# Kernel optimization log

Hardware: AMD Instinct MI355X
Metric: run time of the kernel (lower is better)

## Reference

```python
import jax, jax.numpy as jnp
import numpy as np

KS = 2          # kernel_size
ITERS = 3       # iterations
EPS = 1e-5


def _unfold(x, k):
    # non-overlapping unfold (stride == kernel): (B,C,H,W) -> (B,C,k*k,T)
    B, C, H, W = x.shape
    x = x.reshape(B, C, H // k, k, W // k, k)
    x = x.transpose(0, 1, 3, 5, 2, 4)           # B,C,kh,kw,Ho,Wo
    return x.reshape(B, C, k * k, (H // k) * (W // k))


def _fold(x, H, W, k):
    # inverse of _unfold: (B, C*k*k, T) -> (B,C,H,W)
    B, CKK, T = x.shape
    C = CKK // (k * k)
    x = x.reshape(B, C, k, k, H // k, W // k)
    x = x.transpose(0, 1, 4, 2, 5, 3)            # B,C,Ho,kh,Wo,kw
    return x.reshape(B, C, H, W)


def _ln_channel(x, g, b):
    # LayerNormDim1: LayerNorm over the channel dim (axis=1) of (B,C,H,W)
    mu = jnp.mean(x, axis=1, keepdims=True)
    var = jnp.var(x, axis=1, keepdims=True)
    xn = (x - mu) * jax.lax.rsqrt(var + EPS)
    return xn * g[None, :, None, None] + b[None, :, None, None]


def setup_inputs() -> dict:
    key = jax.random.key(0)
    ks = jax.random.split(key, 7)
    B, f_in, H, W = 4, 256, 128, 128
    f_out = 512
    s = 0.02
    f32 = jnp.float32
    return {
        "x_in": jax.random.normal(ks[0], (B, f_in, H, W), f32),
        "conv_w": jax.random.normal(ks[1], (f_out, f_in, KS, KS), f32) * s,
        "conv_b": jnp.zeros((f_out,), f32),
        "k_w": jax.random.normal(ks[2], (f_out, f_in), f32) * s,
        "k_b": jnp.zeros((f_out,), f32),
        "q_w": jax.random.normal(ks[3], (f_out, f_out), f32) * s,
        "q_b": jnp.zeros((f_out,), f32),
        "v_w": jax.random.normal(ks[4], (f_out, f_in), f32) * s,
        "v_b": jnp.zeros((f_out,), f32),
        "mlp_w": jax.random.normal(ks[5], (f_out, f_out), f32) * s,
        "mlp_b": jnp.zeros((f_out,), f32),
        "lnc_g": jnp.ones((f_out,), f32),
        "lnc_b": jnp.zeros((f_out,), f32),
        "lnv_g": jnp.ones((f_out,), f32),
        "lnv_b": jnp.zeros((f_out,), f32),
        "lnm_g": jnp.ones((f_out,), f32),
        "lnm_b": jnp.zeros((f_out,), f32),
    }


def reference(x_in, conv_w, conv_b, k_w, k_b, q_w, q_b, v_w, v_b,
              mlp_w, mlp_b, lnc_g, lnc_b, lnv_g, lnv_b, lnm_g, lnm_b):
    temp = 1.0
    B, f_in, H, W = x_in.shape
    f_out = conv_w.shape[0]
    WIN = KS * KS
    Ho, Wo = H // KS, W // KS
    T_out = Ho * Wo

    # patchify conv (stride == kernel) + channel LayerNorm
    xc = jax.lax.conv_general_dilated(
        x_in, conv_w, window_strides=(KS, KS), padding="VALID",
        dimension_numbers=("NCHW", "OIHW", "NCHW"))
    x_out = _ln_channel(xc + conv_b[None, :, None, None], lnc_g, lnc_b)

    # k, v projections on the full-resolution input
    k = jnp.einsum("bihw,oi->bohw", x_in, k_w) + k_b[None, :, None, None]
    v = jnp.einsum("bihw,oi->bohw", x_in, v_w) + v_b[None, :, None, None]

    k_wins = _unfold(k, KS)

    for _ in range(ITERS):
        q = jnp.einsum("bihw,oi->bohw", x_out, q_w) + q_b[None, :, None, None]
        q = q.reshape(B, f_out, T_out)
        att = jnp.einsum("bfwt,bft->bwt", k_wins, q)
        att = jax.nn.softmax(att * temp, axis=1)
        att_map = _fold(att, H, W, KS)                   # (B, 1, H, W)
        update = v * att_map                             # broadcast over channels
        update = _unfold(update, KS).sum(axis=2)         # (B, f_out, T_out)
        update = update.reshape(B, f_out, Ho, Wo)
        x_out = x_out + _ln_channel(update, lnv_g, lnv_b)
        mlp = jnp.einsum("bihw,oi->bohw", x_out, mlp_w) + mlp_b[None, :, None, None]
        x_out = x_out + _ln_channel(mlp, lnm_g, lnm_b)

    return x_out
```

## Files before the change

kernel.cpp:

```cpp
#include <hip/hip_runtime.h>

#define NB 4
#define CIN 256
#define CO 512
#define HH 128
#define WW 128
#define PP (HH*WW)
#define HO 64
#define TT (HO*HO)
#define EPSL 1e-5f

typedef unsigned short u16;
typedef unsigned int   u32;
typedef __attribute__((ext_vector_type(8))) short short8;
typedef __attribute__((ext_vector_type(4))) short short4v;
typedef __attribute__((ext_vector_type(4))) float f32x4;

__device__ __forceinline__ float b2f(u16 u){
  union{float f; u32 i;} x; x.i = ((u32)u)<<16; return x.f;
}
__device__ __forceinline__ u16 f2b(float f){
  union{float f; u32 i;} x; x.f = f;
  u32 r = x.i + 0x7fffu + ((x.i>>16)&1u);
  return (u16)(r>>16);
}

__device__ __forceinline__ void gl16(const u16* g, u16* l){
  __builtin_amdgcn_global_load_lds((const __attribute__((address_space(1))) void*)g,
                                   (__attribute__((address_space(3))) void*)l, 16, 0, 0);
}

template<int K, int EPI>
__global__ __launch_bounds__(256) void gemm_t(
    const u16* __restrict__ Ah, const u16* __restrict__ Al, size_t aBS,
    const u16* __restrict__ Bh, const u16* __restrict__ Bl, size_t bBS,
    const float* __restrict__ bias,
    float* __restrict__ OUTf, u16* __restrict__ OPh, u16* __restrict__ OPl,
    size_t oBS, int oLd)
{
  const int z = blockIdx.z;
  const int r0 = blockIdx.x*128, c0 = blockIdx.y*128;
  const int tid = threadIdx.x, wid = tid>>6, lane = tid&63;
  const int wm = wid>>1, wn = wid&1, lr = lane&15, lg = lane>>4;

  extern __shared__ u16 sm[];

  const size_t abase = (size_t)z*aBS + (size_t)r0*K;
  const size_t bbase = (size_t)z*bBS + (size_t)c0*K;

  f32x4 acc[4][4] = {};

  const int q0 = tid, q1 = tid+256;
  const int r_0 = q0>>2, c_0 = q0&3;
  const int r_1 = q1>>2, c_1 = q1&3;
  const size_t go0 = (size_t)r_0*K + (size_t)((c_0 ^ ((r_0>>1)&3))*8);
  const size_t go1 = (size_t)r_1*K + (size_t)((c_1 ^ ((r_1>>1)&3))*8);

  const int NS = K/32;
  #pragma unroll 1
  for (int s = 0; s < NS; ++s) {
    if (s == 0) {
      u16* buf = sm;
      gl16(Ah+abase+go0, buf+q0*8);        gl16(Ah+abase+go1, buf+q1*8);
      gl16(Al+abase+go0, buf+4096+q0*8);   gl16(Al+abase+go1, buf+4096+q1*8);
      gl16(Bh+bbase+go0, buf+8192+q0*8);   gl16(Bh+bbase+go1, buf+8192+q1*8);
      gl16(Bl+bbase+go0, buf+12288+q0*8);  gl16(Bl+bbase+go1, buf+12288+q1*8);
    }
    if (s+1 < NS) {
      u16* buf = sm + ((s+1)&1)*16384;
      const size_t ko = (size_t)(s+1)*32;
      gl16(Ah+abase+go0+ko, buf+q0*8);        gl16(Ah+abase+go1+ko, buf+q1*8);
      gl16(Al+abase+go0+ko, buf+4096+q0*8);   gl16(Al+abase+go1+ko, buf+4096+q1*8);
      gl16(Bh+bbase+go0+ko, buf+8192+q0*8);   gl16(Bh+bbase+go1+ko, buf+8192+q1*8);
      gl16(Bl+bbase+go0+ko, buf+12288+q0*8);  gl16(Bl+bbase+go1+ko, buf+12288+q1*8);
      asm volatile("s_waitcnt vmcnt(8)" ::: "memory");
    } else {
      asm volatile("s_waitcnt vmcnt(0)" ::: "memory");
    }
    __builtin_amdgcn_s_barrier();
    __builtin_amdgcn_sched_barrier(0);
    {
      const u16* buf = sm + (s&1)*16384;
      const u16* Ax = buf, *Ay = buf+4096, *Bx = buf+8192, *By = buf+12288;
      short8 bh[4], bl[4];
      #pragma unroll
      for (int nf=0; nf<4; ++nf) {
        int row = wn*64 + nf*16 + lr;
        int off = row*32 + ((lg ^ ((row>>1)&3))<<3);
        bh[nf] = *(const short8*)(Bx+off);
        bl[nf] = *(const short8*)(By+off);
      }
      #pragma unroll
      for (int mf=0; mf<4; ++mf) {
        int row = wm*64 + mf*16 + lr;
        int off = row*32 + ((lg ^ ((row>>1)&3))<<3);
        short8 ah = *(const short8*)(Ax+off);
        short8 al = *(const short8*)(Ay+off);
        #pragma unroll
        for (int nf=0; nf<4; ++nf) {
          acc[mf][nf] = __builtin_amdgcn_mfma_f32_16x16x32_bf16(ah, bh[nf], acc[mf][nf],0,0,0);
          acc[mf][nf] = __builtin_amdgcn_mfma_f32_16x16x32_bf16(ah, bl[nf], acc[mf][nf],0,0,0);
          acc[mf][nf] = __builtin_amdgcn_mfma_f32_16x16x32_bf16(al, bh[nf], acc[mf][nf],0,0,0);
        }
      }
    }
    __builtin_amdgcn_sched_barrier(0);
    __builtin_amdgcn_s_barrier();
  }
  __builtin_amdgcn_sched_barrier(0);

  #pragma unroll
  for (int mf=0; mf<4; ++mf) {
    #pragma unroll
    for (int nf=0; nf<4; ++nf) {
      int col = c0 + wn*64 + nf*16 + lr;
      #pragma unroll
      for (int j=0; j<4; ++j) {
        int row = r0 + wm*64 + mf*16 + lg*4 + j;
        float v = acc[mf][nf][j] + (EPI==0 ? bias[row] : bias[col]);
        size_t oi = (size_t)z*oBS + (size_t)row*oLd + col;
        if (EPI==0) {
          OUTf[oi] = v;
        } else {
          u16 h = f2b(v);
          OPh[oi] = h;
          OPl[oi] = f2b(v - b2f(h));
        }
      }
    }
  }
}

template<int ADD>
__global__ __launch_bounds__(256) void ln_split(
    const u16* __restrict__ TPh, const u16* __restrict__ TPl,
    const float* __restrict__ g, const float* __restrict__ be,
    u16* __restrict__ XSh, u16* __restrict__ XSl)
{
  const int wid = threadIdx.x>>6, lane = threadIdx.x&63;
  const size_t row = (size_t)blockIdx.x*4 + wid;
  const size_t base = row*CO + lane*8;
  short8 h8 = *(const short8*)(TPh + base);
  short8 l8 = *(const short8*)(TPl + base);
  float v[8]; float s=0.f, s2=0.f;
  #pragma unroll
  for (int e=0;e<8;++e){ v[e]=b2f((u16)h8[e])+b2f((u16)l8[e]); s+=v[e]; s2+=v[e]*v[e]; }
  #pragma unroll
  for (int m=1;m<64;m<<=1){ s+=__shfl_xor(s,m,64); s2+=__shfl_xor(s2,m,64); }
  float mu = s*(1.f/CO);
  float rstd = rsqrtf(s2*(1.f/CO) - mu*mu + EPSL);
  const int cc0 = lane*8;
  float4 g0 = *(const float4*)(g+cc0), g1 = *(const float4*)(g+cc0+4);
  float4 e0 = *(const float4*)(be+cc0), e1 = *(const float4*)(be+cc0+4);
  float gg[8] = {g0.x,g0.y,g0.z,g0.w,g1.x,g1.y,g1.z,g1.w};
  float bb[8] = {e0.x,e0.y,e0.z,e0.w,e1.x,e1.y,e1.z,e1.w};
  short8 xh, xl;
  if (ADD) { xh = *(const short8*)(XSh+base); xl = *(const short8*)(XSl+base); }
  short8 oh, ol;
  #pragma unroll
  for (int e=0;e<8;++e){
    float r = gg[e]*(v[e]-mu)*rstd + bb[e];
    float nv = ADD ? (b2f((u16)xh[e]) + b2f((u16)xl[e]) + r) : r;
    u16 h = f2b(nv); oh[e]=(short)h; ol[e]=(short)f2b(nv - b2f(h));
  }
  *(short8*)(XSh+base) = oh;
  *(short8*)(XSl+base) = ol;
}

__global__ __launch_bounds__(256) void att_xp(
    const float* __restrict__ qk, const float* __restrict__ x_in,
    u16* __restrict__ XPh, u16* __restrict__ XPl)
{
  const int b = blockIdx.y;
  const int tl = threadIdx.x & 63, cg = threadIdx.x >> 6;
  const int t = blockIdx.x*64 + tl;
  const int ho = t >> 6, wo = t & 63;
  const size_t p00 = (size_t)(2*ho)*WW + 2*wo;

  float a0=0.f, a1=0.f, a2=0.f, a3=0.f;
  for (int i = cg*64; i < cg*64 + 64; ++i) {
    float qv = qk[((size_t)b*CIN + i)*TT + t];
    const float* xr = x_in + ((size_t)b*CIN + i)*PP + p00;
    float2 x01 = *(const float2*)xr;
    float2 x23 = *(const float2*)(xr + WW);
    a0 += qv*x01.x; a1 += qv*x01.y; a2 += qv*x23.x; a3 += qv*x23.y;
  }
  __shared__ float attp[4][64][4];
  attp[cg][tl][0] = a0; attp[cg][tl][1] = a1;
  attp[cg][tl][2] = a2; attp[cg][tl][3] = a3;
  __syncthreads();
  a0 = attp[0][tl][0] + attp[1][tl][0] + attp[2][tl][0] + attp[3][tl][0];
  a1 = attp[0][tl][1] + attp[1][tl][1] + attp[2][tl][1] + attp[3][tl][1];
  a2 = attp[0][tl][2] + attp[1][tl][2] + attp[2][tl][2] + attp[3][tl][2];
  a3 = attp[0][tl][3] + attp[1][tl][3] + attp[2][tl][3] + attp[3][tl][3];
  float m = fmaxf(fmaxf(a0,a1), fmaxf(a2,a3));
  float ee0 = __expf(a0-m), ee1 = __expf(a1-m), ee2 = __expf(a2-m), ee3 = __expf(a3-m);
  float inv = 1.f/(ee0+ee1+ee2+ee3);
  float p0 = ee0*inv, p1 = ee1*inv, p2 = ee2*inv, p3 = ee3*inv;

  for (int ib = 0; ib < 64; ib += 8) {
    short8 oh, ol;
    #pragma unroll
    for (int e = 0; e < 8; ++e) {
      int i = cg*64 + ib + e;
      const float* xr = x_in + ((size_t)b*CIN + i)*PP + p00;
      float2 x01 = *(const float2*)xr;
      float2 x23 = *(const float2*)(xr + WW);
      float u = p0*x01.x + p1*x01.y + p2*x23.x + p3*x23.y;
      u16 h = f2b(u); oh[e] = (short)h; ol[e] = (short)f2b(u - b2f(h));
    }
    size_t o = ((size_t)b*TT + t)*CIN + cg*64 + ib;
    *(short8*)(XPh + o) = oh;
    *(short8*)(XPl + o) = ol;
  }
}

__global__ __launch_bounds__(256) void xc_build(
    const float* __restrict__ x_in, u16* __restrict__ XCh, u16* __restrict__ XCl)
{
  const int ho = blockIdx.x, iblk = blockIdx.y, b = blockIdx.z;
  const int tid = threadIdx.x;
  __shared__ float Ls[32][256];
  {
    const int ii = tid >> 3, q = tid & 7;
    const float4* src = (const float4*)(x_in + ((size_t)(b*CIN + iblk*32 + ii)*PP + (size_t)ho*256));
    #pragma unroll
    for (int p = 0; p < 8; ++p) {
      float4 v = src[q + p*8];
      *(float4*)&Ls[ii][(q + p*8)*4] = v;
    }
  }
  __syncthreads();
  {
    const int wo = tid >> 2, w = tid & 3;
    const int colbase = (w>>1)*128 + 2*wo + (w&1);
    u16 hb[32], lb[32];
    #pragma unroll
    for (int ii = 0; ii < 32; ++ii) {
      float v = Ls[ii][colbase];
      u16 h = f2b(v); hb[ii] = h; lb[ii] = f2b(v - b2f(h));
    }
    size_t t = (size_t)b*TT + ho*64 + wo;
    size_t dst = t*1024 + (size_t)w*256 + iblk*32;
    #pragma unroll
    for (int c = 0; c < 4; ++c) {
      short8 hv, lv;
      #pragma unroll
      for (int e = 0; e < 8; ++e) { hv[e] = (short)hb[c*8+e]; lv[e] = (short)lb[c*8+e]; }
      *(short8*)(XCh + dst + c*8) = hv;
      *(short8*)(XCl + dst + c*8) = lv;
    }
  }
}

__global__ __launch_bounds__(256) void out_transpose(
    const u16* __restrict__ XSh, const u16* __restrict__ XSl, float* __restrict__ xout)
{
  const int b = blockIdx.z, c0 = blockIdx.y*64, t0l = blockIdx.x*64;
  const int tid = threadIdx.x;
  __shared__ float Ts[64][68];
  #pragma unroll
  for (int p = 0; p < 2; ++p) {
    int idx = tid + p*256;
    int row = idx >> 3, ko = (idx & 7)*8;
    size_t off = ((size_t)b*TT + t0l + row)*CO + c0 + ko;
    short8 h8 = *(const short8*)(XSh + off);
    short8 l8 = *(const short8*)(XSl + off);
    #pragma unroll
    for (int e = 0; e < 8; ++e)
      Ts[ko + e][row] = b2f((u16)h8[e]) + b2f((u16)l8[e]);
  }
  __syncthreads();
  const int cl = tid >> 2, tq = tid & 3;
  #pragma unroll
  for (int p = 0; p < 4; ++p) {
    int t4 = (tq + p*4)*4;
    float4 v = *(const float4*)&Ts[cl][t4];
    *(float4*)(xout + ((size_t)b*CO + c0 + cl)*TT + t0l + t4) = v;
  }
}

__global__ void split_pack(const float* __restrict__ src, u16* __restrict__ h,
                           u16* __restrict__ l, int n){
  int i = blockIdx.x*256 + threadIdx.x;
  if (i < n) { float v = src[i]; u16 hh = f2b(v); h[i]=hh; l[i]=f2b(v - b2f(hh)); }
}

__global__ void conv_pack(const float* __restrict__ cw, u16* __restrict__ h,
                          u16* __restrict__ l){
  int e = blockIdx.x*256 + threadIdx.x;
  int o = e >> 10, r = e & 1023, w = r >> 8, i = r & 255;
  float v = cw[o*1024 + i*4 + w];
  u16 hh = f2b(v); h[e]=hh; l[e]=f2b(v - b2f(hh));
}

__global__ __launch_bounds__(256) void gemm_tn(
    const float* __restrict__ A, const float* __restrict__ B,
    u16* __restrict__ MtH, u16* __restrict__ MtL)
{
  const int i0 = blockIdx.y*64, j0 = blockIdx.x*64;
  const int tid = threadIdx.x, tx = tid & 15, ty = tid >> 4;
  __shared__ float As[16][64];
  __shared__ float Bs[16][64];
  float acc[4][4] = {};
  for (int f0 = 0; f0 < CO; f0 += 16) {
    int tt = tid & 63, kkb = tid >> 6;
    #pragma unroll
    for (int s = 0; s < 4; ++s) {
      As[kkb+s*4][tt] = A[(size_t)(f0+kkb+s*4)*CIN + i0 + tt];
      Bs[kkb+s*4][tt] = B[(size_t)(f0+kkb+s*4)*CO  + j0 + tt];
    }
    __syncthreads();
    #pragma unroll
    for (int kk = 0; kk < 16; ++kk) {
      float4 av = *reinterpret_cast<const float4*>(&As[kk][ty*4]);
      float4 bv = *reinterpret_cast<const float4*>(&Bs[kk][tx*4]);
      float a[4] = {av.x,av.y,av.z,av.w}, c[4] = {bv.x,bv.y,bv.z,bv.w};
      #pragma unroll
      for (int j = 0; j < 4; ++j)
        #pragma unroll
        for (int i = 0; i < 4; ++i) acc[j][i] += a[j]*c[i];
    }
    __syncthreads();
  }
  #pragma unroll
  for (int j = 0; j < 4; ++j) {
    #pragma unroll
    for (int i = 0; i < 4; ++i) {
      float v = acc[j][i];
      size_t idx = (size_t)(i0+ty*4+j)*CO + j0 + tx*4 + i;
      u16 h = f2b(v);
      MtH[idx] = h; MtL[idx] = f2b(v - b2f(h));
    }
  }
}

__global__ void qbk_kernel(const float* __restrict__ q_b,
                           const float* __restrict__ k_w, float* __restrict__ qbk)
{
  int i = threadIdx.x;
  float s = 0.f;
  for (int f = 0; f < CO; ++f) s += q_b[f]*k_w[(size_t)f*CIN + i];
  qbk[i] = s;
}

extern "C" void kernel_launch(void* const* d_in, const int* in_sizes, int n_in,
                              void* d_out, int out_size, void* d_ws, size_t ws_size,
                              hipStream_t stream) {
  const float* x_in   = (const float*)d_in[0];
  const float* conv_w = (const float*)d_in[1];
  const float* conv_b = (const float*)d_in[2];
  const float* k_w    = (const float*)d_in[3];
  const float* q_w    = (const float*)d_in[5];
  const float* q_b    = (const float*)d_in[6];
  const float* v_w    = (const float*)d_in[7];
  const float* v_b    = (const float*)d_in[8];
  const float* mlp_w  = (const float*)d_in[9];
  const float* mlp_b  = (const float*)d_in[10];
  const float* lnc_g  = (const float*)d_in[11];
  const float* lnc_b  = (const float*)d_in[12];
  const float* lnv_g  = (const float*)d_in[13];
  const float* lnv_b  = (const float*)d_in[14];
  const float* lnm_g  = (const float*)d_in[15];
  const float* lnm_b  = (const float*)d_in[16];
  float* x_out = (float*)d_out;

  char* ws = (char*)d_ws;
  const size_t MBy = (size_t)1<<20;
  u16* XCh = (u16*)(ws + 0*MBy);
  u16* XCl = (u16*)(ws + 32*MBy);
  u16* XSh = (u16*)(ws + 0*MBy);
  u16* XSl = (u16*)(ws + 16*MBy);
  u16* XPh = (u16*)(ws + 32*MBy);
  u16* XPl = (u16*)(ws + 40*MBy);
  float* QK = (float*)(ws + 48*MBy);
  u16* TPh = (u16*)(ws + 64*MBy);
  u16* TPl = (u16*)(ws + 80*MBy);
  u16* WCh = (u16*)(ws + 96*MBy);
  u16* WCl = (u16*)(ws + 97*MBy);
  u16* MWh = (u16*)(ws + 98*MBy);
  u16* MWl = (u16*)(ws + 98*MBy + 512*1024);
  u16* VWh = (u16*)(ws + 99*MBy);
  u16* VWl = (u16*)(ws + 99*MBy + 256*1024);
  u16* MtH = (u16*)(ws + 99*MBy + 512*1024);
  u16* MtL = (u16*)(ws + 99*MBy + 768*1024);
  float* QBK = (float*)(ws + 100*MBy);

  conv_pack<<<2048, 256, 0, stream>>>(conv_w, WCh, WCl);
  split_pack<<<512, 256, 0, stream>>>(v_w, VWh, VWl, CO*CIN);
  split_pack<<<1024, 256, 0, stream>>>(mlp_w, MWh, MWl, CO*CO);
  gemm_tn<<<dim3(CO/64, CIN/64), 256, 0, stream>>>(k_w, q_w, MtH, MtL);
  qbk_kernel<<<1, CIN, 0, stream>>>(q_b, k_w, QBK);
  xc_build<<<dim3(HO, 8, NB), 256, 0, stream>>>(x_in, XCh, XCl);

  gemm_t<1024,1><<<dim3(TT/128, 4, NB), 256, 65536, stream>>>(
      XCh, XCl, (size_t)TT*1024, WCh, WCl, (size_t)0, conv_b,
      nullptr, TPh, TPl, (size_t)TT*CO, CO);
  ln_split<0><<<NB*TT/4, 256, 0, stream>>>(TPh, TPl, lnc_g, lnc_b, XSh, XSl);

  for (int it = 0; it < 3; ++it) {
    gemm_t<512,0><<<dim3(CIN/128, TT/128, NB), 256, 65536, stream>>>(
        MtH, MtL, (size_t)0, XSh, XSl, (size_t)TT*CO, QBK,
        QK, nullptr, nullptr, (size_t)CIN*TT, TT);
    att_xp<<<dim3(TT/64, NB), 256, 0, stream>>>(QK, x_in, XPh, XPl);
    gemm_t<256,1><<<dim3(TT/128, 4, NB), 256, 65536, stream>>>(
        XPh, XPl, (size_t)TT*CIN, VWh, VWl, (size_t)0, v_b,
        nullptr, TPh, TPl, (size_t)TT*CO, CO);
    ln_split<1><<<NB*TT/4, 256, 0, stream>>>(TPh, TPl, lnv_g, lnv_b, XSh, XSl);
    gemm_t<512,1><<<dim3(TT/128, 4, NB), 256, 65536, stream>>>(
        XSh, XSl, (size_t)TT*CO, MWh, MWl, (size_t)0, mlp_b,
        nullptr, TPh, TPl, (size_t)TT*CO, CO);
    ln_split<1><<<NB*TT/4, 256, 0, stream>>>(TPh, TPl, lnm_g, lnm_b, XSh, XSl);
  }

  out_transpose<<<dim3(TT/64, CO/64, NB), 256, 0, stream>>>(XSh, XSl, x_out);
}
```

Measured before the change: 719.0 us.

## Fuse channel LayerNorm into GEMM epilogue with full-row 64x512 tiles

```diff
diff --git a/kernel.cpp b/kernel.cpp
--- a/kernel.cpp
+++ b/kernel.cpp
@@ -8,12 +8,12 @@
 #define PP (HH*WW)
 #define HO 64
 #define TT (HO*HO)
+#define MTOT (NB*TT)
 #define EPSL 1e-5f
 
 typedef unsigned short u16;
 typedef unsigned int   u32;
 typedef __attribute__((ext_vector_type(8))) short short8;
-typedef __attribute__((ext_vector_type(4))) short short4v;
 typedef __attribute__((ext_vector_type(4))) float f32x4;
 
 __device__ __forceinline__ float b2f(u16 u){
@@ -30,13 +30,169 @@
                                    (__attribute__((address_space(3))) void*)l, 16, 0, 0);
 }
 
-template<int K, int EPI>
+template<int K, int MODE>
+__global__ __launch_bounds__(512) void gemm_ln64(
+    const u16* __restrict__ Ah, const u16* __restrict__ Al,
+    const u16* __restrict__ Bh, const u16* __restrict__ Bl,
+    const float* __restrict__ bias,
+    const float* __restrict__ g, const float* __restrict__ be,
+    u16* __restrict__ XSh, u16* __restrict__ XSl)
+{
+  const int r0 = blockIdx.x*64;
+  const int tid = threadIdx.x, wid = tid>>6, lane = tid&63;
+  const int lr = lane&15, lg = lane>>4;
+
+  __shared__ u16 smAh[2][2048];
+  __shared__ u16 smAl[2][2048];
+  __shared__ u16 smBh[2][16384];
+  __shared__ u16 smBl[2][16384];
+  __shared__ float red[2][64][8];
+
+  const size_t abase = (size_t)r0*K;
+  f32x4 acc[4][4] = {};
+
+  const int ach = tid & 255;
+  const int ar = ach>>2, ac = ach&3;
+  const size_t agoff = (size_t)ar*K + (size_t)((ac ^ ((ar>>1)&3))*8);
+  const u16* Aptr = (tid < 256 ? Ah : Al);
+  int brow[4]; size_t bgoff[4];
+  #pragma unroll
+  for (int p=0;p<4;++p){
+    int cb = p*512 + tid;
+    brow[p] = cb>>2; int bc = cb&3;
+    bgoff[p] = (size_t)brow[p]*K + (size_t)((bc ^ ((brow[p]>>1)&3))*8);
+  }
+
+  const int NS = K/32;
+  #pragma unroll 1
+  for (int s = 0; s < NS; ++s) {
+    if (s == 0) {
+      u16* a_d = (tid<256 ? smAh[0] : smAl[0]);
+      gl16(Aptr+abase+agoff, a_d + ach*8);
+      #pragma unroll
+      for (int p=0;p<4;++p){
+        int cb = p*512 + tid;
+        gl16(Bh+bgoff[p], smBh[0] + cb*8);
+        gl16(Bl+bgoff[p], smBl[0] + cb*8);
+      }
+    }
+    if (s+1 < NS) {
+      const int nb = (s+1)&1;
+      const size_t ko = (size_t)(s+1)*32;
+      u16* a_d = (tid<256 ? smAh[nb] : smAl[nb]);
+      gl16(Aptr+abase+agoff+ko, a_d + ach*8);
+      #pragma unroll
+      for (int p=0;p<4;++p){
+        int cb = p*512 + tid;
+        gl16(Bh+bgoff[p]+ko, smBh[nb] + cb*8);
+        gl16(Bl+bgoff[p]+ko, smBl[nb] + cb*8);
+      }
+      asm volatile("s_waitcnt vmcnt(9)" ::: "memory");
+    } else {
+      asm volatile("s_waitcnt vmcnt(0)" ::: "memory");
+    }
+    __builtin_amdgcn_s_barrier();
+    __builtin_amdgcn_sched_barrier(0);
+    {
+      const int bs = s&1;
+      short8 bhf[4], blf[4];
+      #pragma unroll
+      for (int nf=0; nf<4; ++nf) {
+        int row = wid*64 + nf*16 + lr;
+        int off = row*32 + ((lg ^ ((row>>1)&3))<<3);
+        bhf[nf] = *(const short8*)(smBh[bs]+off);
+        blf[nf] = *(const short8*)(smBl[bs]+off);
+      }
+      #pragma unroll
+      for (int mf=0; mf<4; ++mf) {
+        int row = mf*16 + lr;
+        int off = row*32 + ((lg ^ ((row>>1)&3))<<3);
+        short8 ah = *(const short8*)(smAh[bs]+off);
+        short8 al = *(const short8*)(smAl[bs]+off);
+        #pragma unroll
+        for (int nf=0; nf<4; ++nf) {
+          acc[mf][nf] = __builtin_amdgcn_mfma_f32_16x16x32_bf16(ah, bhf[nf], acc[mf][nf],0,0,0);
+          acc[mf][nf] = __builtin_amdgcn_mfma_f32_16x16x32_bf16(ah, blf[nf], acc[mf][nf],0,0,0);
+          acc[mf][nf] = __builtin_amdgcn_mfma_f32_16x16x32_bf16(al, bhf[nf], acc[mf][nf],0,0,0);
+        }
+      }
+    }
+    __builtin_amdgcn_sched_barrier(0);
+    __builtin_amdgcn_s_barrier();
+  }
+  __builtin_amdgcn_sched_barrier(0);
+
+  float s1[4][4] = {}, s2v[4][4] = {};
+  #pragma unroll
+  for (int nf=0; nf<4; ++nf) {
+    float bs = bias[wid*64 + nf*16 + lr];
+    #pragma unroll
+    for (int mf=0; mf<4; ++mf)
+      #pragma unroll
+      for (int j=0; j<4; ++j) {
+        float v = acc[mf][nf][j] + bs;
+        acc[mf][nf][j] = v;
+        s1[mf][j] += v; s2v[mf][j] += v*v;
+      }
+  }
+  #pragma unroll
+  for (int m=1; m<=8; m<<=1)
+    #pragma unroll
+    for (int mf=0; mf<4; ++mf)
+      #pragma unroll
+      for (int j=0; j<4; ++j) {
+        s1[mf][j]  += __shfl_xor(s1[mf][j],  m, 64);
+        s2v[mf][j] += __shfl_xor(s2v[mf][j], m, 64);
+      }
+  if (lr == 0) {
+    #pragma unroll
+    for (int mf=0; mf<4; ++mf)
+      #pragma unroll
+      for (int j=0; j<4; ++j) {
+        int row = mf*16 + lg*4 + j;
+        red[0][row][wid] = s1[mf][j];
+        red[1][row][wid] = s2v[mf][j];
+      }
+  }
+  __syncthreads();
+  float mu[4][4], rs[4][4];
+  #pragma unroll
+  for (int mf=0; mf<4; ++mf)
+    #pragma unroll
+    for (int j=0; j<4; ++j) {
+      int row = mf*16 + lg*4 + j;
+      float S = 0.f, S2 = 0.f;
+      #pragma unroll
+      for (int w=0; w<8; ++w) { S += red[0][row][w]; S2 += red[1][row][w]; }
+      float m_ = S*(1.f/CO);
+      mu[mf][j] = m_;
+      rs[mf][j] = rsqrtf(S2*(1.f/CO) - m_*m_ + EPSL);
+    }
+  #pragma unroll
+  for (int nf=0; nf<4; ++nf) {
+    int col = wid*64 + nf*16 + lr;
+    float gg = g[col], bb = be[col];
+    #pragma unroll
+    for (int mf=0; mf<4; ++mf)
+      #pragma unroll
+      for (int j=0; j<4; ++j) {
+        size_t grow = (size_t)r0 + mf*16 + lg*4 + j;
+        size_t xi = grow*CO + col;
+        float r = gg*(acc[mf][nf][j]-mu[mf][j])*rs[mf][j] + bb;
+        float nv = MODE ? (b2f(XSh[xi]) + b2f(XSl[xi]) + r) : r;
+        u16 h = f2b(nv);
+        XSh[xi] = h;
+        XSl[xi] = f2b(nv - b2f(h));
+      }
+  }
+}
+
+template<int K>
 __global__ __launch_bounds__(256) void gemm_t(
     const u16* __restrict__ Ah, const u16* __restrict__ Al, size_t aBS,
     const u16* __restrict__ Bh, const u16* __restrict__ Bl, size_t bBS,
     const float* __restrict__ bias,
-    float* __restrict__ OUTf, u16* __restrict__ OPh, u16* __restrict__ OPl,
-    size_t oBS, int oLd)
+    float* __restrict__ OUTf, size_t oBS, int oLd)
 {
   const int z = blockIdx.z;
   const int r0 = blockIdx.x*128, c0 = blockIdx.y*128;
@@ -117,54 +273,10 @@
       #pragma unroll
       for (int j=0; j<4; ++j) {
         int row = r0 + wm*64 + mf*16 + lg*4 + j;
-        float v = acc[mf][nf][j] + (EPI==0 ? bias[row] : bias[col]);
-        size_t oi = (size_t)z*oBS + (size_t)row*oLd + col;
-        if (EPI==0) {
-          OUTf[oi] = v;
-        } else {
-          u16 h = f2b(v);
-          OPh[oi] = h;
-          OPl[oi] = f2b(v - b2f(h));
-        }
-      }
-    }
-  }
-}
-
-template<int ADD>
-__global__ __launch_bounds__(256) void ln_split(
-    const u16* __restrict__ TPh, const u16* __restrict__ TPl,
-    const float* __restrict__ g, const float* __restrict__ be,
-    u16* __restrict__ XSh, u16* __restrict__ XSl)
-{
-  const int wid = threadIdx.x>>6, lane = threadIdx.x&63;
-  const size_t row = (size_t)blockIdx.x*4 + wid;
-  const size_t base = row*CO + lane*8;
-  short8 h8 = *(const short8*)(TPh + base);
-  short8 l8 = *(const short8*)(TPl + base);
-  float v[8]; float s=0.f, s2=0.f;
-  #pragma unroll
-  for (int e=0;e<8;++e){ v[e]=b2f((u16)h8[e])+b2f((u16)l8[e]); s+=v[e]; s2+=v[e]*v[e]; }
-  #pragma unroll
-  for (int m=1;m<64;m<<=1){ s+=__shfl_xor(s,m,64); s2+=__shfl_xor(s2,m,64); }
-  float mu = s*(1.f/CO);
-  float rstd = rsqrtf(s2*(1.f/CO) - mu*mu + EPSL);
-  const int cc0 = lane*8;
-  float4 g0 = *(const float4*)(g+cc0), g1 = *(const float4*)(g+cc0+4);
-  float4 e0 = *(const float4*)(be+cc0), e1 = *(const float4*)(be+cc0+4);
-  float gg[8] = {g0.x,g0.y,g0.z,g0.w,g1.x,g1.y,g1.z,g1.w};
-  float bb[8] = {e0.x,e0.y,e0.z,e0.w,e1.x,e1.y,e1.z,e1.w};
-  short8 xh, xl;
-  if (ADD) { xh = *(const short8*)(XSh+base); xl = *(const short8*)(XSl+base); }
-  short8 oh, ol;
-  #pragma unroll
-  for (int e=0;e<8;++e){
-    float r = gg[e]*(v[e]-mu)*rstd + bb[e];
-    float nv = ADD ? (b2f((u16)xh[e]) + b2f((u16)xl[e]) + r) : r;
-    u16 h = f2b(nv); oh[e]=(short)h; ol[e]=(short)f2b(nv - b2f(h));
-  }
-  *(short8*)(XSh+base) = oh;
-  *(short8*)(XSl+base) = ol;
+        OUTf[(size_t)z*oBS + (size_t)row*oLd + col] = acc[mf][nf][j] + bias[row];
+      }
+    }
+  }
 }
 
 __global__ __launch_bounds__(256) void att_xp(
@@ -369,22 +481,20 @@
   const size_t MBy = (size_t)1<<20;
   u16* XCh = (u16*)(ws + 0*MBy);
   u16* XCl = (u16*)(ws + 32*MBy);
-  u16* XSh = (u16*)(ws + 0*MBy);
-  u16* XSl = (u16*)(ws + 16*MBy);
-  u16* XPh = (u16*)(ws + 32*MBy);
-  u16* XPl = (u16*)(ws + 40*MBy);
-  float* QK = (float*)(ws + 48*MBy);
-  u16* TPh = (u16*)(ws + 64*MBy);
-  u16* TPl = (u16*)(ws + 80*MBy);
-  u16* WCh = (u16*)(ws + 96*MBy);
-  u16* WCl = (u16*)(ws + 97*MBy);
-  u16* MWh = (u16*)(ws + 98*MBy);
-  u16* MWl = (u16*)(ws + 98*MBy + 512*1024);
-  u16* VWh = (u16*)(ws + 99*MBy);
-  u16* VWl = (u16*)(ws + 99*MBy + 256*1024);
-  u16* MtH = (u16*)(ws + 99*MBy + 512*1024);
-  u16* MtL = (u16*)(ws + 99*MBy + 768*1024);
-  float* QBK = (float*)(ws + 100*MBy);
+  u16* XSh = (u16*)(ws + 64*MBy);
+  u16* XSl = (u16*)(ws + 80*MBy);
+  u16* XPh = (u16*)(ws + 96*MBy);
+  u16* XPl = (u16*)(ws + 104*MBy);
+  float* QK = (float*)(ws + 112*MBy);
+  u16* WCh = (u16*)(ws + 128*MBy);
+  u16* WCl = (u16*)(ws + 129*MBy);
+  u16* MWh = (u16*)(ws + 130*MBy);
+  u16* MWl = (u16*)(ws + 130*MBy + 512*1024);
+  u16* VWh = (u16*)(ws + 131*MBy);
+  u16* VWl = (u16*)(ws + 131*MBy + 256*1024);
+  u16* MtH = (u16*)(ws + 131*MBy + 512*1024);
+  u16* MtL = (u16*)(ws + 131*MBy + 768*1024);
+  float* QBK = (float*)(ws + 132*MBy);
 
   conv_pack<<<2048, 256, 0, stream>>>(conv_w, WCh, WCl);
   split_pack<<<512, 256, 0, stream>>>(v_w, VWh, VWl, CO*CIN);
@@ -393,24 +503,18 @@
   qbk_kernel<<<1, CIN, 0, stream>>>(q_b, k_w, QBK);
   xc_build<<<dim3(HO, 8, NB), 256, 0, stream>>>(x_in, XCh, XCl);
 
-  gemm_t<1024,1><<<dim3(TT/128, 4, NB), 256, 65536, stream>>>(
-      XCh, XCl, (size_t)TT*1024, WCh, WCl, (size_t)0, conv_b,
-      nullptr, TPh, TPl, (size_t)TT*CO, CO);
-  ln_split<0><<<NB*TT/4, 256, 0, stream>>>(TPh, TPl, lnc_g, lnc_b, XSh, XSl);
+  gemm_ln64<1024,0><<<MTOT/64, 512, 0, stream>>>(
+      XCh, XCl, WCh, WCl, conv_b, lnc_g, lnc_b, XSh, XSl);
 
   for (int it = 0; it < 3; ++it) {
-    gemm_t<512,0><<<dim3(CIN/128, TT/128, NB), 256, 65536, stream>>>(
+    gemm_t<512><<<dim3(CIN/128, TT/128, NB), 256, 65536, stream>>>(
         MtH, MtL, (size_t)0, XSh, XSl, (size_t)TT*CO, QBK,
-        QK, nullptr, nullptr, (size_t)CIN*TT, TT);
+        QK, (size_t)CIN*TT, TT);
     att_xp<<<dim3(TT/64, NB), 256, 0, stream>>>(QK, x_in, XPh, XPl);
-    gemm_t<256,1><<<dim3(TT/128, 4, NB), 256, 65536, stream>>>(
-        XPh, XPl, (size_t)TT*CIN, VWh, VWl, (size_t)0, v_b,
-        nullptr, TPh, TPl, (size_t)TT*CO, CO);
-    ln_split<1><<<NB*TT/4, 256, 0, stream>>>(TPh, TPl, lnv_g, lnv_b, XSh, XSl);
-    gemm_t<512,1><<<dim3(TT/128, 4, NB), 256, 65536, stream>>>(
-        XSh, XSl, (size_t)TT*CO, MWh, MWl, (size_t)0, mlp_b,
-        nullptr, TPh, TPl, (size_t)TT*CO, CO);
-    ln_split<1><<<NB*TT/4, 256, 0, stream>>>(TPh, TPl, lnm_g, lnm_b, XSh, XSl);
+    gemm_ln64<256,1><<<MTOT/64, 512, 0, stream>>>(
+        XPh, XPl, VWh, VWl, v_b, lnv_g, lnv_b, XSh, XSl);
+    gemm_ln64<512,1><<<MTOT/64, 512, 0, stream>>>(
+        XSh, XSl, MWh, MWl, mlp_b, lnm_g, lnm_b, XSh, XSl);
   }
 
   out_transpose<<<dim3(TT/64, CO/64, NB), 256, 0, stream>>>(XSh, XSl, x_out);
```

New measurement: 811.5 us. 1.13x slower.
